# Optimization experiments

Measured on AMD Instinct MI355X. Metric: run time of the kernel, lower is better.

## Reference

```python
import jax, jax.numpy as jnp
import numpy as np

N, L, S, D, H = 4, 8192, 8192, 256, 8
DH = D // H  # 32
EPS_ATTN = 1e-6
EPS_LN = 1e-5


def setup_inputs() -> dict:
    key = jax.random.key(0)
    ks = jax.random.split(key, 8)
    w = lambda k, sh: jax.random.normal(k, sh, jnp.float32) * 0.02
    return {
        "x": jax.random.normal(ks[0], (N, L, D), jnp.float32),
        "source": jax.random.normal(ks[1], (N, S, D), jnp.float32),
        "Wq": w(ks[2], (D, D)),
        "Wk": w(ks[3], (D, D)),
        "Wv": w(ks[4], (D, D)),
        "Wm": w(ks[5], (D, D)),
        "W1": w(ks[6], (2 * D, 2 * D)),
        "W2": w(ks[7], (2 * D, D)),
        "g1": jnp.ones((D,), jnp.float32),
        "b1": jnp.zeros((D,), jnp.float32),
        "g2": jnp.ones((D,), jnp.float32),
        "b2": jnp.zeros((D,), jnp.float32),
    }


def _layernorm(x, g, b):
    m = jnp.mean(x, axis=-1, keepdims=True)
    v = jnp.var(x, axis=-1, keepdims=True)
    return (x - m) * jax.lax.rsqrt(v + EPS_LN) * g + b


def reference(x, source, Wq, Wk, Wv, Wm, W1, W2, g1, b1, g2, b2):
    bs = x.shape[0]
    # QKV projections (bias=False), split heads -> [N, L/S, H, DH]
    q = (x @ Wq).reshape(bs, -1, H, DH)
    k = (source @ Wk).reshape(bs, -1, H, DH)
    v = (source @ Wv).reshape(bs, -1, H, DH)
    # elu+1 feature map (linear attention, LoFTR-style)
    Q = jax.nn.elu(q) + 1.0
    K = jax.nn.elu(k) + 1.0
    v_len = v.shape[1]
    vals = v / v_len
    KV = jnp.einsum("nshd,nshv->nhdv", K, vals)  # [N, H, DH, DH]
    Z = 1.0 / (jnp.einsum("nlhd,nhd->nlh", Q, K.sum(axis=1)) + EPS_ATTN)
    msg = jnp.einsum("nlhd,nhdv,nlh->nlhv", Q, KV, Z) * v_len  # [N, L, H, DH]
    # merge heads + LN
    msg = msg.reshape(bs, -1, H * DH) @ Wm
    msg = _layernorm(msg, g1, b1)
    # concat-MLP with LeakyReLU(0.1)
    h = jnp.concatenate([x, msg], axis=2) @ W1
    h = jnp.where(h >= 0, h, 0.1 * h)
    msg = h @ W2
    msg = _layernorm(msg, g2, b2)
    return x + msg
```

## Files before the change

kernel.cpp:

```cpp
#include <hip/hip_runtime.h>

typedef __bf16 bf16;
typedef __bf16 bf16x4 __attribute__((ext_vector_type(4)));
typedef __bf16 bf16x8 __attribute__((ext_vector_type(8)));
typedef float f32x4 __attribute__((ext_vector_type(4)));

__device__ __forceinline__ float apply_epi(float v, int epi) {
  if (epi == 1) return v > 0.f ? v + 1.f : __expf(v);
  if (epi == 2) return v >= 0.f ? v : 0.1f * v;
  return v;
}

__device__ __forceinline__ void g2l16(const bf16* gp, bf16* lp) {
  __builtin_amdgcn_global_load_lds(
      (const __attribute__((address_space(1))) void*)gp,
      (__attribute__((address_space(3))) void*)lp, 16, 0, 0);
}

__global__ void detect_kernel(const unsigned* g1raw, int* flag) {
  if (threadIdx.x == 0 && blockIdx.x == 0)
    *flag = (g1raw[0] == 0x3F800000u) ? 1 : 0;
}

struct TransArgs {
  const void* src[6];
  bf16* dst[6];
  int R[6], C[6], t0[6];
};

__global__ __launch_bounds__(256) void prep_kernel(
    const void* __restrict__ xin, const void* __restrict__ sin,
    bf16* __restrict__ bx, bf16* __restrict__ bs,
    TransArgs ta, const int* flagp) {
  const bool f32 = (*flagp != 0);
  if (blockIdx.x < 8192) {
    const void* s;
    bf16* d;
    size_t i;
    if (blockIdx.x < 4096) {
      s = xin; d = bx; i = (size_t)blockIdx.x * 2048 + threadIdx.x * 8;
    } else {
      s = sin; d = bs; i = (size_t)(blockIdx.x - 4096) * 2048 + threadIdx.x * 8;
    }
    if (f32) {
      f32x4 lo = *(const f32x4*)((const float*)s + i);
      f32x4 hi = *(const f32x4*)((const float*)s + i + 4);
      bf16x8 t;
      t[0] = (bf16)lo[0]; t[1] = (bf16)lo[1]; t[2] = (bf16)lo[2]; t[3] = (bf16)lo[3];
      t[4] = (bf16)hi[0]; t[5] = (bf16)hi[1]; t[6] = (bf16)hi[2]; t[7] = (bf16)hi[3];
      *(bf16x8*)(d + i) = t;
    } else {
      *(bf16x8*)(d + i) = *(const bf16x8*)((const bf16*)s + i);
    }
    return;
  }
  __shared__ bf16 tile[32][33];
  int bid = blockIdx.x - 8192;
  int si = 0;
#pragma unroll
  for (int i = 1; i < 6; ++i)
    if (bid >= ta.t0[i]) si = i;
  const void* srcv = ta.src[si];
  bf16* dst = ta.dst[si];
  int R = ta.R[si], Cc = ta.C[si];
  int lt = bid - ta.t0[si];
  int tpr = Cc >> 5;
  int tr = lt / tpr, tc = lt % tpr;
  int tx = threadIdx.x & 31, ty0 = threadIdx.x >> 5;
#pragma unroll
  for (int i = 0; i < 4; ++i) {
    int ty = ty0 + i * 8;
    size_t idx = (size_t)(tr * 32 + ty) * Cc + tc * 32 + tx;
    tile[ty][tx] = f32 ? (bf16)((const float*)srcv)[idx] : ((const bf16*)srcv)[idx];
  }
  __syncthreads();
#pragma unroll
  for (int i = 0; i < 4; ++i) {
    int ty = ty0 + i * 8;
    dst[(size_t)(tc * 32 + ty) * R + tr * 32 + tx] = tile[tx][ty];
  }
}

#define TM 256
#define TN 256
#define TK 64

__global__ __launch_bounds__(512, 2) void gemm256(
    const bf16* __restrict__ A, const bf16* __restrict__ A2, int ldA,
    const bf16* __restrict__ Bt, bf16* __restrict__ C, int Nn, int Kk, int epi,
    bf16* __restrict__ C2, int epi2, int split, int gridM) {
  __shared__ bf16 lds[2][2][2][128 * 64];
  const int tid = threadIdx.x;

  const int nwg = gridDim.x;
  const int cpx = nwg >> 3;
  const int swz = (blockIdx.x & 7) * cpx + (blockIdx.x >> 3);
  const int mb = swz % gridM, nb = swz / gridM;
  const int m0 = mb * TM, n0 = nb * TN;

  const int wave = tid >> 6, lane = tid & 63;
  const int wm = (wave >> 2) * 128, wn = (wave & 3) * 64;
  const int q = lane >> 4, mr = lane & 15;
  const int ahalf = wm >> 7, bhalf = wn >> 7;
  const int bro = wn & 64;

  const int kTiles = Kk / TK;

  f32x4 acc[8][4];
#pragma unroll
  for (int i = 0; i < 8; ++i)
#pragma unroll
    for (int j = 0; j < 4; ++j) acc[i][j] = (f32x4){0.f, 0.f, 0.f, 0.f};

  auto stageA = [&](int t, int half) {
    const bf16* Ab = A;
    int kcol = t * TK;
    if (A2 && kcol >= 256) { Ab = A2; kcol -= 256; }
    bf16* dst = &lds[t & 1][0][half][0];
#pragma unroll
    for (int ld = 0; ld < 2; ++ld) {
      int id = ld * 512 + tid;
      int rr = id >> 3, pp = id & 7, gg = pp ^ (rr & 7);
      g2l16(Ab + (size_t)(m0 + half * 128 + rr) * ldA + kcol + gg * 8, dst + id * 8);
    }
  };
  auto stageB = [&](int t, int half) {
    bf16* dst = &lds[t & 1][1][half][0];
    int kk = t * TK;
#pragma unroll
    for (int ld = 0; ld < 2; ++ld) {
      int id = ld * 512 + tid;
      int rr = id >> 3, pp = id & 7, gg = pp ^ (rr & 7);
      g2l16(Bt + (size_t)(n0 + half * 128 + rr) * Kk + kk + gg * 8, dst + id * 8);
    }
  };

  bf16x8 af[8], bfr[8];
  auto rdA = [&](const bf16* base, int mlo) {
#pragma unroll
    for (int i = 0; i < 4; ++i) {
      int r = (mlo + i) * 16 + mr;
#pragma unroll
      for (int ks = 0; ks < 2; ++ks)
        af[i * 2 + ks] = *(const bf16x8*)&base[r * TK + (((ks * 4 + q) ^ (r & 7)) * 8)];
    }
  };
  auto rdB = [&](bf16x8* bo, const bf16* base, int nlo) {
#pragma unroll
    for (int i = 0; i < 2; ++i) {
      int r = bro + (nlo + i) * 16 + mr;
#pragma unroll
      for (int ks = 0; ks < 2; ++ks)
        bo[i * 2 + ks] = *(const bf16x8*)&base[r * TK + (((ks * 4 + q) ^ (r & 7)) * 8)];
    }
  };
  auto mma = [&](const bf16x8* bo, int mlo, int nlo) {
    __builtin_amdgcn_s_setprio(1);
#pragma unroll
    for (int i = 0; i < 4; ++i)
#pragma unroll
      for (int j = 0; j < 2; ++j)
#pragma unroll
        for (int ks = 0; ks < 2; ++ks)
          acc[mlo + i][nlo + j] = __builtin_amdgcn_mfma_f32_16x16x32_bf16(
              af[i * 2 + ks], bo[j * 2 + ks], acc[mlo + i][nlo + j], 0, 0, 0);
    __builtin_amdgcn_s_setprio(0);
  };

#define PH_END asm volatile("s_waitcnt lgkmcnt(0)\n\ts_barrier" ::: "memory")
#define PH_END_VM asm volatile("s_waitcnt vmcnt(4) lgkmcnt(0)\n\ts_barrier" ::: "memory")
#define PH_END_VM0 asm volatile("s_waitcnt vmcnt(0) lgkmcnt(0)\n\ts_barrier" ::: "memory")

  stageB(0, 0); stageB(0, 1); stageA(0, 0); stageA(0, 1); stageB(1, 0); stageB(1, 1);
  asm volatile("s_waitcnt vmcnt(4)\n\ts_barrier" ::: "memory");

  const bf16* A0 = &lds[0][0][ahalf][0];
  const bf16* B0 = &lds[0][1][bhalf][0];
  const bf16* A1 = &lds[1][0][ahalf][0];
  const bf16* B1 = &lds[1][1][bhalf][0];

  const int nIter = kTiles >> 1;
  for (int p = 0; p < nIter - 1; ++p) {
    const int t0 = 2 * p, t1 = 2 * p + 1;
    rdA(A0, 0); rdB(bfr + 0, B0, 0);
    stageA(t1, 0);
    mma(bfr + 0, 0, 0);
    PH_END;
    rdB(bfr + 4, B0, 2);
    stageA(t1, 1);
    mma(bfr + 4, 0, 2);
    PH_END;
    rdA(A0, 4);
    stageB(t0 + 2, 0);
    mma(bfr + 0, 4, 0);
    PH_END;
    stageB(t0 + 2, 1);
    mma(bfr + 4, 4, 2);
    PH_END_VM;
    rdA(A1, 0); rdB(bfr + 0, B1, 0);
    stageA(t0 + 2, 0);
    mma(bfr + 0, 0, 0);
    PH_END;
    rdB(bfr + 4, B1, 2);
    stageA(t0 + 2, 1);
    mma(bfr + 4, 0, 2);
    PH_END;
    rdA(A1, 4);
    stageB(t1 + 2, 0);
    mma(bfr + 0, 4, 0);
    PH_END;
    stageB(t1 + 2, 1);
    mma(bfr + 4, 4, 2);
    PH_END_VM;
  }
  {
    const int t1 = kTiles - 1;
    rdA(A0, 0); rdB(bfr + 0, B0, 0);
    stageA(t1, 0);
    mma(bfr + 0, 0, 0);
    PH_END;
    rdB(bfr + 4, B0, 2);
    stageA(t1, 1);
    mma(bfr + 4, 0, 2);
    PH_END;
    rdA(A0, 4);
    mma(bfr + 0, 4, 0);
    PH_END;
    mma(bfr + 4, 4, 2);
    PH_END_VM0;
    rdA(A1, 0); rdB(bfr + 0, B1, 0);
    mma(bfr + 0, 0, 0);
    PH_END;
    rdB(bfr + 4, B1, 2);
    mma(bfr + 4, 0, 2);
    PH_END;
    rdA(A1, 4);
    mma(bfr + 0, 4, 0);
    PH_END;
    mma(bfr + 4, 4, 2);
    asm volatile("s_waitcnt lgkmcnt(0)" ::: "memory");
  }
#undef PH_END
#undef PH_END_VM
#undef PH_END_VM0

  bf16* Cw = C;
  int nbase = n0, ep = epi;
  if (C2 && n0 >= split) { Cw = C2; nbase = n0 - split; ep = epi2; }
#pragma unroll
  for (int mi = 0; mi < 8; ++mi)
#pragma unroll
    for (int ni = 0; ni < 4; ++ni)
#pragma unroll
      for (int r4 = 0; r4 < 4; ++r4) {
        int row = m0 + wm + mi * 16 + q * 4 + r4;
        int cn = nbase + wn + ni * 16 + mr;
        float v = apply_epi(acc[mi][ni][r4], ep);
        Cw[(size_t)row * Nn + cn] = (bf16)v;
      }
}

#define KVCH 256
__global__ __launch_bounds__(256) void kv_kernel(
    const bf16* __restrict__ Kf, const bf16* __restrict__ V,
    float* __restrict__ partial, float* __restrict__ pk) {
  __shared__ bf16 Ks[KVCH][32];
  __shared__ bf16 Vs[KVCH][32];
  const int cb = blockIdx.x, h = blockIdx.y, n = blockIdx.z;
  const int tid = threadIdx.x;
  const int wave = tid >> 6, lane = tid & 63;
  const int d0 = (lane & 7) * 4, dv0 = (lane >> 3) * 4;
  const int s0 = cb * KVCH;
#pragma unroll
  for (int rd = 0; rd < 4; ++rd) {
    int rr = rd * 64 + (tid >> 2), pp = tid & 3;
    size_t g = ((size_t)(n * 8192 + s0 + rr)) * 256 + h * 32 + pp * 8;
    *(bf16x8*)&Ks[rr][pp * 8] = *(const bf16x8*)(Kf + g);
    *(bf16x8*)&Vs[rr][pp * 8] = *(const bf16x8*)(V + g);
  }
  __syncthreads();
  float acc[4][4] = {};
  float ks4[4] = {};
#pragma unroll 4
  for (int si = 0; si < 64; ++si) {
    int s = wave * 64 + si;
    bf16x4 k4 = *(const bf16x4*)&Ks[s][d0];
    bf16x4 v4 = *(const bf16x4*)&Vs[s][dv0];
    float kf[4] = {(float)k4[0], (float)k4[1], (float)k4[2], (float)k4[3]};
    float vf[4] = {(float)v4[0], (float)v4[1], (float)v4[2], (float)v4[3]};
#pragma unroll
    for (int vi = 0; vi < 4; ++vi)
#pragma unroll
      for (int di = 0; di < 4; ++di) acc[vi][di] = fmaf(vf[vi], kf[di], acc[vi][di]);
#pragma unroll
    for (int di = 0; di < 4; ++di) ks4[di] += kf[di];
  }
  __syncthreads();
  float* red = (float*)&Ks[0][0];
  float* ksr = (float*)&Vs[0][0];
#pragma unroll
  for (int vi = 0; vi < 4; ++vi)
#pragma unroll
    for (int di = 0; di < 4; ++di)
      red[wave * 1024 + (dv0 + vi) * 32 + d0 + di] = acc[vi][di];
  if (dv0 == 0) {
#pragma unroll
    for (int di = 0; di < 4; ++di) ksr[wave * 32 + d0 + di] = ks4[di];
  }
  __syncthreads();
  const size_t slot = (size_t)(n * 8 + h) * 32 + cb;
  f32x4 s4 = {0.f, 0.f, 0.f, 0.f};
#pragma unroll
  for (int w = 0; w < 4; ++w) s4 += *(const f32x4*)&red[w * 1024 + tid * 4];
  *(f32x4*)&partial[slot * 1024 + tid * 4] = s4;
  if (tid < 32) {
    float ss = 0.f;
#pragma unroll
    for (int w = 0; w < 4; ++w) ss += ksr[w * 32 + tid];
    pk[slot * 32 + tid] = ss;
  }
}

__global__ __launch_bounds__(256) void kv_reduce(
    const float* __restrict__ partial, const float* __restrict__ pk,
    float* __restrict__ kv_acc, float* __restrict__ ksum) {
  const int b = blockIdx.x;
  const int t = threadIdx.x;
  f32x4 s4 = {0.f, 0.f, 0.f, 0.f};
  for (int c = 0; c < 32; ++c)
    s4 += *(const f32x4*)&partial[((size_t)b * 32 + c) * 1024 + t * 4];
  *(f32x4*)&kv_acc[(size_t)b * 1024 + t * 4] = s4;
  if (t < 32) {
    float ss = 0.f;
    for (int c = 0; c < 32; ++c) ss += pk[((size_t)b * 32 + c) * 32 + t];
    ksum[(size_t)b * 32 + t] = ss;
  }
}

__global__ __launch_bounds__(256) void msg_kernel(
    const bf16* __restrict__ Q, const float* __restrict__ kv_acc,
    const float* __restrict__ ksum, bf16* __restrict__ msg) {
  __shared__ bf16 kvt[8][32][32];
  __shared__ float ksl[8][32];
  __shared__ float zl[8][128];
  int tid = threadIdx.x;
  int row0 = blockIdx.x * 128;
  int n = row0 >> 13;
  const float* kvb = kv_acc + (size_t)n * 8192;
  for (int i = tid; i < 8192; i += 256) ((bf16*)kvt)[i] = (bf16)kvb[i];
  ((float*)ksl)[tid] = ksum[(size_t)n * 256 + tid];
  __syncthreads();
  int r = tid & 127, hg = tid >> 7;
  const bf16* qrow = Q + (size_t)(row0 + r) * 256;
#pragma unroll
  for (int hh = 0; hh < 4; ++hh) {
    int h = hg * 4 + hh;
    float dot = 0.f;
#pragma unroll
    for (int d = 0; d < 32; ++d) dot = fmaf((float)qrow[h * 32 + d], ksl[h][d], dot);
    zl[h][r] = 1.f / (dot + 1e-6f);
  }
  __syncthreads();
  int wave = tid >> 6, lane = tid & 63, q = lane >> 4, mr = lane & 15;
  f32x4 zero = {0.f, 0.f, 0.f, 0.f};
  for (int h = 0; h < 8; ++h) {
    bf16x8 b0 = *(const bf16x8*)&kvt[h][mr][q * 8];
    bf16x8 b1 = *(const bf16x8*)&kvt[h][16 + mr][q * 8];
#pragma unroll
    for (int mi = 0; mi < 2; ++mi) {
      int arow = wave * 32 + mi * 16 + mr;
      bf16x8 a = *(const bf16x8*)(Q + (size_t)(row0 + arow) * 256 + h * 32 + q * 8);
      f32x4 c0 = __builtin_amdgcn_mfma_f32_16x16x32_bf16(a, b0, zero, 0, 0, 0);
      f32x4 c1 = __builtin_amdgcn_mfma_f32_16x16x32_bf16(a, b1, zero, 0, 0, 0);
#pragma unroll
      for (int r4 = 0; r4 < 4; ++r4) {
        int orow = wave * 32 + mi * 16 + q * 4 + r4;
        float z = zl[h][orow];
        size_t ob = (size_t)(row0 + orow) * 256 + h * 32;
        msg[ob + mr] = (bf16)(c0[r4] * z);
        msg[ob + 16 + mr] = (bf16)(c1[r4] * z);
      }
    }
  }
}

__global__ __launch_bounds__(256) void ln_kernel(
    const bf16* __restrict__ in, const void* __restrict__ g, const void* __restrict__ b,
    const void* __restrict__ resid, void* __restrict__ outp,
    const int* flagp, int ioDual) {
  const bool gbF32 = (*flagp != 0);
  const bool ioF32 = ioDual && gbF32;
  int wave = threadIdx.x >> 6, lane = threadIdx.x & 63;
  size_t row = (size_t)blockIdx.x * 4 + wave;
  int c = lane * 4;
  bf16x4 v = *(const bf16x4*)(in + row * 256 + c);
  float x0 = (float)v[0], x1 = (float)v[1], x2 = (float)v[2], x3 = (float)v[3];
  float s = x0 + x1 + x2 + x3;
  float sq = x0 * x0 + x1 * x1 + x2 * x2 + x3 * x3;
#pragma unroll
  for (int o = 32; o > 0; o >>= 1) {
    s += __shfl_xor(s, o);
    sq += __shfl_xor(sq, o);
  }
  float mean = s * (1.f / 256.f);
  float var = sq * (1.f / 256.f) - mean * mean;
  float rstd = rsqrtf(var + 1e-5f);
  float g0, g1v, g2v, g3, b0, b1v, b2v, b3;
  if (gbF32) {
    f32x4 gv = *(const f32x4*)((const float*)g + c);
    f32x4 bv = *(const f32x4*)((const float*)b + c);
    g0 = gv[0]; g1v = gv[1]; g2v = gv[2]; g3 = gv[3];
    b0 = bv[0]; b1v = bv[1]; b2v = bv[2]; b3 = bv[3];
  } else {
    bf16x4 gv = *(const bf16x4*)((const bf16*)g + c);
    bf16x4 bv = *(const bf16x4*)((const bf16*)b + c);
    g0 = (float)gv[0]; g1v = (float)gv[1]; g2v = (float)gv[2]; g3 = (float)gv[3];
    b0 = (float)bv[0]; b1v = (float)bv[1]; b2v = (float)bv[2]; b3 = (float)bv[3];
  }
  float y0 = (x0 - mean) * rstd * g0 + b0;
  float y1 = (x1 - mean) * rstd * g1v + b1v;
  float y2 = (x2 - mean) * rstd * g2v + b2v;
  float y3 = (x3 - mean) * rstd * g3 + b3;
  if (resid) {
    if (ioF32) {
      f32x4 rv = *(const f32x4*)((const float*)resid + row * 256 + c);
      y0 += rv[0]; y1 += rv[1]; y2 += rv[2]; y3 += rv[3];
    } else {
      bf16x4 rv = *(const bf16x4*)((const bf16*)resid + row * 256 + c);
      y0 += (float)rv[0]; y1 += (float)rv[1]; y2 += (float)rv[2]; y3 += (float)rv[3];
    }
  }
  if (ioF32) {
    f32x4 o4 = {y0, y1, y2, y3};
    *(f32x4*)((float*)outp + row * 256 + c) = o4;
  } else {
    bf16x4 o4;
    o4[0] = (bf16)y0; o4[1] = (bf16)y1; o4[2] = (bf16)y2; o4[3] = (bf16)y3;
    *(bf16x4*)((bf16*)outp + row * 256 + c) = o4;
  }
}

extern "C" void kernel_launch(void* const* d_in, const int* in_sizes, int n_in,
                              void* d_out, int out_size, void* d_ws, size_t ws_size,
                              hipStream_t stream) {
  const void* x   = d_in[0];
  const void* src = d_in[1];
  const void* Wq  = d_in[2];
  const void* Wk  = d_in[3];
  const void* Wv  = d_in[4];
  const void* Wm  = d_in[5];
  const void* W1  = d_in[6];
  const void* W2  = d_in[7];
  const void* g1  = d_in[8];
  const void* b1  = d_in[9];
  const void* g2  = d_in[10];
  const void* b2  = d_in[11];

  char* ws = (char*)d_ws;
  bf16* bufA = (bf16*)(ws);
  bf16* bufB = (bf16*)(ws + ((size_t)16 << 20));
  bf16* bufC = (bf16*)(ws + ((size_t)32 << 20));
  bf16* WqT  = (bf16*)(ws + ((size_t)48 << 20));
  bf16* WkvT = WqT + 65536;
  bf16* WmT  = WkvT + 131072;
  bf16* W1T  = WmT + 65536;
  bf16* W2T  = W1T + 262144;
  float* kv_acc = (float*)(ws + ((size_t)50 << 20));
  float* ksum = kv_acc + 32768;
  int* flagp = (int*)(ws + ((size_t)50 << 20) + 160 * 1024);
  float* partial = (float*)(ws + ((size_t)51 << 20));
  float* pk = (float*)(ws + ((size_t)55 << 20));
  bf16* bufX = (bf16*)d_out;
  bf16* bufS = bufX + 8388608;

  detect_kernel<<<dim3(1), dim3(64), 0, stream>>>((const unsigned*)g1, flagp);

  TransArgs ta;
  ta.src[0] = Wq; ta.src[1] = Wk; ta.src[2] = Wv; ta.src[3] = Wm; ta.src[4] = W1; ta.src[5] = W2;
  ta.dst[0] = WqT; ta.dst[1] = WkvT; ta.dst[2] = WkvT + 65536; ta.dst[3] = WmT; ta.dst[4] = W1T; ta.dst[5] = W2T;
  ta.R[0] = 256; ta.R[1] = 256; ta.R[2] = 256; ta.R[3] = 256; ta.R[4] = 512; ta.R[5] = 512;
  ta.C[0] = 256; ta.C[1] = 256; ta.C[2] = 256; ta.C[3] = 256; ta.C[4] = 512; ta.C[5] = 256;
  ta.t0[0] = 0; ta.t0[1] = 64; ta.t0[2] = 128; ta.t0[3] = 192; ta.t0[4] = 256; ta.t0[5] = 512;
  prep_kernel<<<dim3(8832), dim3(256), 0, stream>>>(x, src, bufX, bufS, ta, flagp);

  gemm256<<<dim3(128), dim3(512), 0, stream>>>(bufX, nullptr, 256, WqT, bufA, 256, 256, 1,
                                               nullptr, 0, 0, 128);
  gemm256<<<dim3(256), dim3(512), 0, stream>>>(bufS, nullptr, 256, WkvT, bufB, 256, 256, 1,
                                               bufC, 0, 256, 128);

  kv_kernel<<<dim3(32, 8, 4), dim3(256), 0, stream>>>(bufB, bufC, partial, pk);
  kv_reduce<<<dim3(32), dim3(256), 0, stream>>>(partial, pk, kv_acc, ksum);

  msg_kernel<<<dim3(256), dim3(256), 0, stream>>>(bufA, kv_acc, ksum, bufB);

  gemm256<<<dim3(128), dim3(512), 0, stream>>>(bufB, nullptr, 256, WmT, bufA, 256, 256, 0,
                                               nullptr, 0, 0, 128);

  ln_kernel<<<dim3(8192), dim3(256), 0, stream>>>(bufA, g1, b1, nullptr, bufC, flagp, 0);

  gemm256<<<dim3(256), dim3(512), 0, stream>>>(bufX, bufC, 256, W1T, bufA, 512, 512, 2,
                                               nullptr, 0, 0, 128);

  gemm256<<<dim3(128), dim3(512), 0, stream>>>(bufA, nullptr, 512, W2T, bufC, 256, 512, 0,
                                               nullptr, 0, 0, 128);

  ln_kernel<<<dim3(8192), dim3(256), 0, stream>>>(bufC, g2, b2, x, d_out, flagp, 1);
}
```

Before: 292.6 us.

## Fuse LayerNorm into GEMM epilogues and merge QKV GEMMs into one launch

Merges the Q and K/V projection GEMMs into a single 384-block launch so all three jobs share one wave of workgroups. It folds both LayerNorms into the epilogues of the Wm and W2 GEMMs, using an LDS scratch reduction across the four column waves, and adds the residual directly in the second one. The dtype detect kernel is dropped in favour of an inline check on g1. This removes two LN kernel launches, the bf16 intermediate round-trips through memory, and extra launch overhead. In exchange it adds an LDS reduction and barrier in the GEMM epilogue, and the epilogue stores stay scalar.

```diff
diff --git a/kernel.cpp b/kernel.cpp
--- a/kernel.cpp
+++ b/kernel.cpp
@@ -17,10 +17,7 @@
       (__attribute__((address_space(3))) void*)lp, 16, 0, 0);
 }
 
-__global__ void detect_kernel(const unsigned* g1raw, int* flag) {
-  if (threadIdx.x == 0 && blockIdx.x == 0)
-    *flag = (g1raw[0] == 0x3F800000u) ? 1 : 0;
-}
+__device__ __forceinline__ bool is_f32(const unsigned* w) { return w[0] == 0x3F800000u; }
 
 struct TransArgs {
   const void* src[6];
@@ -31,8 +28,8 @@
 __global__ __launch_bounds__(256) void prep_kernel(
     const void* __restrict__ xin, const void* __restrict__ sin,
     bf16* __restrict__ bx, bf16* __restrict__ bs,
-    TransArgs ta, const int* flagp) {
-  const bool f32 = (*flagp != 0);
+    TransArgs ta, const unsigned* __restrict__ g1w) {
+  const bool f32 = is_f32(g1w);
   if (blockIdx.x < 8192) {
     const void* s;
     bf16* d;
@@ -81,23 +78,12 @@
   }
 }
 
-#define TM 256
-#define TN 256
 #define TK 64
 
-__global__ __launch_bounds__(512, 2) void gemm256(
+__device__ __forceinline__ void gemm_core(
     const bf16* __restrict__ A, const bf16* __restrict__ A2, int ldA,
-    const bf16* __restrict__ Bt, bf16* __restrict__ C, int Nn, int Kk, int epi,
-    bf16* __restrict__ C2, int epi2, int split, int gridM) {
-  __shared__ bf16 lds[2][2][2][128 * 64];
-  const int tid = threadIdx.x;
-
-  const int nwg = gridDim.x;
-  const int cpx = nwg >> 3;
-  const int swz = (blockIdx.x & 7) * cpx + (blockIdx.x >> 3);
-  const int mb = swz % gridM, nb = swz / gridM;
-  const int m0 = mb * TM, n0 = nb * TN;
-
+    const bf16* __restrict__ Bt, int Kk, int m0, int n0,
+    bf16 (&lds)[2][2][2][128 * 64], f32x4 (&acc)[8][4], int tid) {
   const int wave = tid >> 6, lane = tid & 63;
   const int wm = (wave >> 2) * 128, wn = (wave & 3) * 64;
   const int q = lane >> 4, mr = lane & 15;
@@ -105,12 +91,6 @@
   const int bro = wn & 64;
 
   const int kTiles = Kk / TK;
-
-  f32x4 acc[8][4];
-#pragma unroll
-  for (int i = 0; i < 8; ++i)
-#pragma unroll
-    for (int j = 0; j < 4; ++j) acc[i][j] = (f32x4){0.f, 0.f, 0.f, 0.f};
 
   auto stageA = [&](int t, int half) {
     const bf16* Ab = A;
@@ -243,10 +223,34 @@
 #undef PH_END
 #undef PH_END_VM
 #undef PH_END_VM0
-
-  bf16* Cw = C;
-  int nbase = n0, ep = epi;
-  if (C2 && n0 >= split) { Cw = C2; nbase = n0 - split; ep = epi2; }
+}
+
+__global__ __launch_bounds__(512, 2) void gemm_qkv(
+    const bf16* __restrict__ Ax, const bf16* __restrict__ As_,
+    const bf16* __restrict__ BtQ, const bf16* __restrict__ BtKV,
+    bf16* __restrict__ Cq, bf16* __restrict__ Ck, bf16* __restrict__ Cv) {
+  __shared__ bf16 lds[2][2][2][128 * 64];
+  const int tid = threadIdx.x;
+  const int swz = ((int)blockIdx.x & 7) * 48 + ((int)blockIdx.x >> 3);
+  const int job = swz / 128, jb = swz % 128;
+  const int m0 = jb * 256;
+
+  const bf16* Ap; const bf16* Btp; bf16* Cp; int ep;
+  if (job == 0)      { Ap = Ax;  Btp = BtQ;          Cp = Cq; ep = 1; }
+  else if (job == 1) { Ap = As_; Btp = BtKV;         Cp = Ck; ep = 1; }
+  else               { Ap = As_; Btp = BtKV + 65536; Cp = Cv; ep = 0; }
+
+  f32x4 acc[8][4];
+#pragma unroll
+  for (int i = 0; i < 8; ++i)
+#pragma unroll
+    for (int j = 0; j < 4; ++j) acc[i][j] = (f32x4){0.f, 0.f, 0.f, 0.f};
+
+  gemm_core(Ap, nullptr, 256, Btp, 256, m0, 0, lds, acc, tid);
+
+  const int wave = tid >> 6, lane = tid & 63;
+  const int wm = (wave >> 2) * 128, wn = (wave & 3) * 64;
+  const int q = lane >> 4, mr = lane & 15;
 #pragma unroll
   for (int mi = 0; mi < 8; ++mi)
 #pragma unroll
@@ -254,9 +258,130 @@
 #pragma unroll
       for (int r4 = 0; r4 < 4; ++r4) {
         int row = m0 + wm + mi * 16 + q * 4 + r4;
-        int cn = nbase + wn + ni * 16 + mr;
-        float v = apply_epi(acc[mi][ni][r4], ep);
-        Cw[(size_t)row * Nn + cn] = (bf16)v;
+        int cn = wn + ni * 16 + mr;
+        Cp[(size_t)row * 256 + cn] = (bf16)apply_epi(acc[mi][ni][r4], ep);
+      }
+}
+
+__global__ __launch_bounds__(512, 2) void gemm_ln(
+    const bf16* __restrict__ A, int ldA, const bf16* __restrict__ Bt, int Kk,
+    const void* __restrict__ gptr, const void* __restrict__ bptr,
+    const void* __restrict__ resid, void* __restrict__ outp, bf16* __restrict__ Cout,
+    const unsigned* __restrict__ g1w, int mode) {
+  __shared__ bf16 lds[2][2][2][128 * 64];
+  const int tid = threadIdx.x;
+  const int swz = ((int)blockIdx.x & 7) * 16 + ((int)blockIdx.x >> 3);
+  const int m0 = swz * 256;
+
+  f32x4 acc[8][4];
+#pragma unroll
+  for (int i = 0; i < 8; ++i)
+#pragma unroll
+    for (int j = 0; j < 4; ++j) acc[i][j] = (f32x4){0.f, 0.f, 0.f, 0.f};
+
+  gemm_core(A, nullptr, ldA, Bt, Kk, m0, 0, lds, acc, tid);
+
+  const int wave = tid >> 6, lane = tid & 63;
+  const int wm = (wave >> 2) * 128, wn = (wave & 3) * 64;
+  const int q = lane >> 4, mr = lane & 15;
+  const int wq = wave & 3;
+  const bool f32io = is_f32(g1w);
+
+  float* scr = (float*)&lds[0][0][0][0];
+  __syncthreads();
+#pragma unroll
+  for (int mi = 0; mi < 8; ++mi)
+#pragma unroll
+    for (int r4 = 0; r4 < 4; ++r4) {
+      float v0 = acc[mi][0][r4], v1 = acc[mi][1][r4], v2 = acc[mi][2][r4], v3 = acc[mi][3][r4];
+      float s = v0 + v1 + v2 + v3;
+      float sq = v0 * v0 + v1 * v1 + v2 * v2 + v3 * v3;
+#pragma unroll
+      for (int o = 1; o < 16; o <<= 1) {
+        s += __shfl_xor(s, o);
+        sq += __shfl_xor(sq, o);
+      }
+      if (mr == 0) {
+        int row = wm + mi * 16 + q * 4 + r4;
+        scr[row * 8 + wq * 2 + 0] = s;
+        scr[row * 8 + wq * 2 + 1] = sq;
+      }
+    }
+  __syncthreads();
+
+  float gv[4], bv[4];
+#pragma unroll
+  for (int ni = 0; ni < 4; ++ni) {
+    int col = wn + ni * 16 + mr;
+    if (f32io) {
+      gv[ni] = ((const float*)gptr)[col];
+      bv[ni] = ((const float*)bptr)[col];
+    } else {
+      gv[ni] = (float)((const bf16*)gptr)[col];
+      bv[ni] = (float)((const bf16*)bptr)[col];
+    }
+  }
+
+#pragma unroll
+  for (int mi = 0; mi < 8; ++mi)
+#pragma unroll
+    for (int r4 = 0; r4 < 4; ++r4) {
+      int row = wm + mi * 16 + q * 4 + r4;
+      float S = scr[row * 8 + 0] + scr[row * 8 + 2] + scr[row * 8 + 4] + scr[row * 8 + 6];
+      float SQ = scr[row * 8 + 1] + scr[row * 8 + 3] + scr[row * 8 + 5] + scr[row * 8 + 7];
+      float mean = S * (1.f / 256.f);
+      float var = SQ * (1.f / 256.f) - mean * mean;
+      float rstd = rsqrtf(var + 1e-5f);
+#pragma unroll
+      for (int ni = 0; ni < 4; ++ni) {
+        int col = wn + ni * 16 + mr;
+        float y = (acc[mi][ni][r4] - mean) * rstd * gv[ni] + bv[ni];
+        size_t off = (size_t)(m0 + row) * 256 + col;
+        if (mode == 0) {
+          Cout[off] = (bf16)y;
+        } else {
+          if (f32io) {
+            ((float*)outp)[off] = y + ((const float*)resid)[off];
+          } else {
+            ((bf16*)outp)[off] = (bf16)(y + (float)((const bf16*)resid)[off]);
+          }
+        }
+      }
+    }
+}
+
+__global__ __launch_bounds__(512, 2) void gemm256(
+    const bf16* __restrict__ A, const bf16* __restrict__ A2, int ldA,
+    const bf16* __restrict__ Bt, bf16* __restrict__ C, int Nn, int Kk, int epi,
+    int gridM) {
+  __shared__ bf16 lds[2][2][2][128 * 64];
+  const int tid = threadIdx.x;
+  const int nwg = gridDim.x;
+  const int cpx = nwg >> 3;
+  const int swz = ((int)blockIdx.x & 7) * cpx + ((int)blockIdx.x >> 3);
+  const int mb = swz % gridM, nb = swz / gridM;
+  const int m0 = mb * 256, n0 = nb * 256;
+
+  f32x4 acc[8][4];
+#pragma unroll
+  for (int i = 0; i < 8; ++i)
+#pragma unroll
+    for (int j = 0; j < 4; ++j) acc[i][j] = (f32x4){0.f, 0.f, 0.f, 0.f};
+
+  gemm_core(A, A2, ldA, Bt, Kk, m0, n0, lds, acc, tid);
+
+  const int wave = tid >> 6, lane = tid & 63;
+  const int wm = (wave >> 2) * 128, wn = (wave & 3) * 64;
+  const int q = lane >> 4, mr = lane & 15;
+#pragma unroll
+  for (int mi = 0; mi < 8; ++mi)
+#pragma unroll
+    for (int ni = 0; ni < 4; ++ni)
+#pragma unroll
+      for (int r4 = 0; r4 < 4; ++r4) {
+        int row = m0 + wm + mi * 16 + q * 4 + r4;
+        int cn = n0 + wn + ni * 16 + mr;
+        C[(size_t)row * Nn + cn] = (bf16)apply_epi(acc[mi][ni][r4], epi);
       }
 }
 
@@ -381,62 +506,6 @@
         msg[ob + 16 + mr] = (bf16)(c1[r4] * z);
       }
     }
-  }
-}
-
-__global__ __launch_bounds__(256) void ln_kernel(
-    const bf16* __restrict__ in, const void* __restrict__ g, const void* __restrict__ b,
-    const void* __restrict__ resid, void* __restrict__ outp,
-    const int* flagp, int ioDual) {
-  const bool gbF32 = (*flagp != 0);
-  const bool ioF32 = ioDual && gbF32;
-  int wave = threadIdx.x >> 6, lane = threadIdx.x & 63;
-  size_t row = (size_t)blockIdx.x * 4 + wave;
-  int c = lane * 4;
-  bf16x4 v = *(const bf16x4*)(in + row * 256 + c);
-  float x0 = (float)v[0], x1 = (float)v[1], x2 = (float)v[2], x3 = (float)v[3];
-  float s = x0 + x1 + x2 + x3;
-  float sq = x0 * x0 + x1 * x1 + x2 * x2 + x3 * x3;
-#pragma unroll
-  for (int o = 32; o > 0; o >>= 1) {
-    s += __shfl_xor(s, o);
-    sq += __shfl_xor(sq, o);
-  }
-  float mean = s * (1.f / 256.f);
-  float var = sq * (1.f / 256.f) - mean * mean;
-  float rstd = rsqrtf(var + 1e-5f);
-  float g0, g1v, g2v, g3, b0, b1v, b2v, b3;
-  if (gbF32) {
-    f32x4 gv = *(const f32x4*)((const float*)g + c);
-    f32x4 bv = *(const f32x4*)((const float*)b + c);
-    g0 = gv[0]; g1v = gv[1]; g2v = gv[2]; g3 = gv[3];
-    b0 = bv[0]; b1v = bv[1]; b2v = bv[2]; b3 = bv[3];
-  } else {
-    bf16x4 gv = *(const bf16x4*)((const bf16*)g + c);
-    bf16x4 bv = *(const bf16x4*)((const bf16*)b + c);
-    g0 = (float)gv[0]; g1v = (float)gv[1]; g2v = (float)gv[2]; g3 = (float)gv[3];
-    b0 = (float)bv[0]; b1v = (float)bv[1]; b2v = (float)bv[2]; b3 = (float)bv[3];
-  }
-  float y0 = (x0 - mean) * rstd * g0 + b0;
-  float y1 = (x1 - mean) * rstd * g1v + b1v;
-  float y2 = (x2 - mean) * rstd * g2v + b2v;
-  float y3 = (x3 - mean) * rstd * g3 + b3;
-  if (resid) {
-    if (ioF32) {
-      f32x4 rv = *(const f32x4*)((const float*)resid + row * 256 + c);
-      y0 += rv[0]; y1 += rv[1]; y2 += rv[2]; y3 += rv[3];
-    } else {
-      bf16x4 rv = *(const bf16x4*)((const bf16*)resid + row * 256 + c);
-      y0 += (float)rv[0]; y1 += (float)rv[1]; y2 += (float)rv[2]; y3 += (float)rv[3];
-    }
-  }
-  if (ioF32) {
-    f32x4 o4 = {y0, y1, y2, y3};
-    *(f32x4*)((float*)outp + row * 256 + c) = o4;
-  } else {
-    bf16x4 o4;
-    o4[0] = (bf16)y0; o4[1] = (bf16)y1; o4[2] = (bf16)y2; o4[3] = (bf16)y3;
-    *(bf16x4*)((bf16*)outp + row * 256 + c) = o4;
   }
 }
 
@@ -467,13 +536,10 @@
   bf16* W2T  = W1T + 262144;
   float* kv_acc = (float*)(ws + ((size_t)50 << 20));
   float* ksum = kv_acc + 32768;
-  int* flagp = (int*)(ws + ((size_t)50 << 20) + 160 * 1024);
   float* partial = (float*)(ws + ((size_t)51 << 20));
   float* pk = (float*)(ws + ((size_t)55 << 20));
   bf16* bufX = (bf16*)d_out;
   bf16* bufS = bufX + 8388608;
-
-  detect_kernel<<<dim3(1), dim3(64), 0, stream>>>((const unsigned*)g1, flagp);
 
   TransArgs ta;
   ta.src[0] = Wq; ta.src[1] = Wk; ta.src[2] = Wv; ta.src[3] = Wm; ta.src[4] = W1; ta.src[5] = W2;
@@ -481,28 +547,20 @@
   ta.R[0] = 256; ta.R[1] = 256; ta.R[2] = 256; ta.R[3] = 256; ta.R[4] = 512; ta.R[5] = 512;
   ta.C[0] = 256; ta.C[1] = 256; ta.C[2] = 256; ta.C[3] = 256; ta.C[4] = 512; ta.C[5] = 256;
   ta.t0[0] = 0; ta.t0[1] = 64; ta.t0[2] = 128; ta.t0[3] = 192; ta.t0[4] = 256; ta.t0[5] = 512;
-  prep_kernel<<<dim3(8832), dim3(256), 0, stream>>>(x, src, bufX, bufS, ta, flagp);
-
-  gemm256<<<dim3(128), dim3(512), 0, stream>>>(bufX, nullptr, 256, WqT, bufA, 256, 256, 1,
-                                               nullptr, 0, 0, 128);
-  gemm256<<<dim3(256), dim3(512), 0, stream>>>(bufS, nullptr, 256, WkvT, bufB, 256, 256, 1,
-                                               bufC, 0, 256, 128);
+  prep_kernel<<<dim3(8832), dim3(256), 0, stream>>>(x, src, bufX, bufS, ta, (const unsigned*)g1);
+
+  gemm_qkv<<<dim3(384), dim3(512), 0, stream>>>(bufX, bufS, WqT, WkvT, bufA, bufB, bufC);
 
   kv_kernel<<<dim3(32, 8, 4), dim3(256), 0, stream>>>(bufB, bufC, partial, pk);
   kv_reduce<<<dim3(32), dim3(256), 0, stream>>>(partial, pk, kv_acc, ksum);
 
   msg_kernel<<<dim3(256), dim3(256), 0, stream>>>(bufA, kv_acc, ksum, bufB);
 
-  gemm256<<<dim3(128), dim3(512), 0, stream>>>(bufB, nullptr, 256, WmT, bufA, 256, 256, 0,
-                                               nullptr, 0, 0, 128);
-
-  ln_kernel<<<dim3(8192), dim3(256), 0, stream>>>(bufA, g1, b1, nullptr, bufC, flagp, 0);
-
-  gemm256<<<dim3(256), dim3(512), 0, stream>>>(bufX, bufC, 256, W1T, bufA, 512, 512, 2,
-                                               nullptr, 0, 0, 128);
-
-  gemm256<<<dim3(128), dim3(512), 0, stream>>>(bufA, nullptr, 512, W2T, bufC, 256, 512, 0,
-                                               nullptr, 0, 0, 128);
-
-  ln_kernel<<<dim3(8192), dim3(256), 0, stream>>>(bufC, g2, b2, x, d_out, flagp, 1);
-}
+  gemm_ln<<<dim3(128), dim3(512), 0, stream>>>(bufB, 256, WmT, 256, g1, b1,
+                                               nullptr, nullptr, bufC, (const unsigned*)g1, 0);
+
+  gemm256<<<dim3(256), dim3(512), 0, stream>>>(bufX, bufC, 256, W1T, bufA, 512, 512, 2, 128);
+
+  gemm_ln<<<dim3(128), dim3(512), 0, stream>>>(bufA, 512, W2T, 512, g2, b2,
+                                               x, d_out, nullptr, (const unsigned*)g1, 1);
+}
```

New measurement: 445.6 us. +52.3%, slower.
